# Optimization experiments

Measured on AMD Instinct MI355X. Metric: run time of the kernel, lower is better.

Reference implementation:

```python
import jax, jax.numpy as jnp
import numpy as np

L, D, H, HK, HD, FF = 4, 1024, 16, 8, 64, 3072
WIN = 12          # sliding_window from Krop.__init__
THETA = 1e6       # Qwen3 rope_theta
EPS = 1e-6


def rmsnorm(x, w):
    return x * jax.lax.rsqrt(jnp.mean(x * x, axis=-1, keepdims=True) + EPS) * w


def rope_cos_sin(S):
    inv = 1.0 / (THETA ** (jnp.arange(0, HD, 2, dtype=jnp.float32) / HD))
    ang = jnp.arange(S, dtype=jnp.float32)[:, None] * inv[None, :]  # [S, HD/2]
    emb = jnp.concatenate([ang, ang], axis=-1)                      # [S, HD]
    return jnp.cos(emb), jnp.sin(emb)


def rotate_half(x):
    a, b = jnp.split(x, 2, axis=-1)
    return jnp.concatenate([-b, a], axis=-1)


def apply_rope(x, cos, sin):
    # x: [B,S,h,HD]; cos/sin: [S,HD]
    return x * cos[None, :, None, :] + rotate_half(x) * sin[None, :, None, :]


def setup_inputs() -> dict:
    key = jax.random.key(0)
    ks = jax.random.split(key, 9)
    s = 0.02
    B, S = 4, 1024
    return {
        "inputs_embeds": jax.random.normal(ks[0], (B, S, D), jnp.float32),
        "wq": jax.random.normal(ks[1], (L, D, H * HD), jnp.float32) * s,
        "wk": jax.random.normal(ks[2], (L, D, HK * HD), jnp.float32) * s,
        "wv": jax.random.normal(ks[3], (L, D, HK * HD), jnp.float32) * s,
        "wo": jax.random.normal(ks[4], (L, H * HD, D), jnp.float32) * s,
        "q_norm_w": jnp.ones((L, HD), jnp.float32),
        "k_norm_w": jnp.ones((L, HD), jnp.float32),
        "ln1_w": jnp.ones((L, D), jnp.float32),
        "ln2_w": jnp.ones((L, D), jnp.float32),
        "w_gate": jax.random.normal(ks[5], (L, D, FF), jnp.float32) * s,
        "w_up": jax.random.normal(ks[6], (L, D, FF), jnp.float32) * s,
        "w_down": jax.random.normal(ks[7], (L, FF, D), jnp.float32) * s,
        "norm_w": jnp.ones((D,), jnp.float32),
        "attention_mask": jnp.ones((B, S), jnp.int32),
    }


def reference(inputs_embeds, wq, wk, wv, wo, q_norm_w, k_norm_w, ln1_w, ln2_w,
              w_gate, w_up, w_down, norm_w, attention_mask):
    B, S, _ = inputs_embeds.shape
    pad = attention_mask > 0                                   # [B,S] key-padding
    # _prepare_4d_attention_mask(...) == 0 -> True where attended (NON-causal)
    full_mask = pad[:, None, None, :]                          # [B,1,1,S]
    idx = jnp.arange(S)
    band = jnp.abs(idx[:, None] - idx[None, :]) <= WIN         # tril(triu(.,-W),W)
    sliding_mask = full_mask & band[None, None, :, :]          # [B,1,S,S]

    cos, sin = rope_cos_sin(S)
    scale = 1.0 / np.sqrt(HD)
    neg = jnp.finfo(inputs_embeds.dtype).min

    h = inputs_embeds
    for l in range(L):
        # layer_types alternate: even -> full_attention, odd -> sliding_attention
        mask = full_mask if l % 2 == 0 else sliding_mask
        n = rmsnorm(h, ln1_w[l])
        q = (n @ wq[l]).reshape(B, S, H, HD)
        k = (n @ wk[l]).reshape(B, S, HK, HD)
        v = (n @ wv[l]).reshape(B, S, HK, HD)
        q = apply_rope(rmsnorm(q, q_norm_w[l]), cos, sin)
        k = apply_rope(rmsnorm(k, k_norm_w[l]), cos, sin)
        k = jnp.repeat(k, H // HK, axis=2)                     # GQA expand
        v = jnp.repeat(v, H // HK, axis=2)
        scores = jnp.einsum('bqhd,bkhd->bhqk', q, k) * scale   # eager full scores
        scores = jnp.where(mask, scores, neg)
        p = jax.nn.softmax(scores, axis=-1)
        ctx = jnp.einsum('bhqk,bkhd->bqhd', p, v).reshape(B, S, H * HD)
        h = h + ctx @ wo[l]
        n2 = rmsnorm(h, ln2_w[l])
        h = h + (jax.nn.silu(n2 @ w_gate[l]) * (n2 @ w_up[l])) @ w_down[l]
    return rmsnorm(h, norm_w)
```

## Files before the change

### kernel.cpp

```cpp
#include <hip/hip_runtime.h>

typedef unsigned short u16;
typedef __attribute__((ext_vector_type(8))) short bf16x8;
typedef __attribute__((ext_vector_type(4))) float f32x4;

__device__ __forceinline__ u16 f2bf(float x){
  union { float f; unsigned u; } v; v.f = x;
  unsigned r = v.u + 0x7FFFu + ((v.u >> 16) & 1u);
  return (u16)(r >> 16);
}
__device__ __forceinline__ float bf2f(u16 x){
  union { unsigned u; float f; } v; v.u = ((unsigned)x) << 16;
  return v.f;
}
__device__ __forceinline__ void async16(const u16* g, u16* l){
  __builtin_amdgcn_global_load_lds((const __attribute__((address_space(1))) void*)g,
                                   (__attribute__((address_space(3))) void*)l, 16, 0, 0);
}

__global__ __launch_bounds__(256) void k_transpose_cvt(
    const float* __restrict__ in, u16* __restrict__ out,
    int R, int C, size_t in_ls, size_t out_ls, int c_off){
  __shared__ float tile[32][33];
  in  += (size_t)blockIdx.z * in_ls;
  out += (size_t)blockIdx.z * out_ls;
  int c0 = blockIdx.x * 32 + c_off, r0 = blockIdx.y * 32;
  int tx = threadIdx.x & 31, ty = threadIdx.x >> 5;
  #pragma unroll
  for (int i = 0; i < 32; i += 8)
    tile[ty + i][tx] = in[(size_t)(r0 + ty + i) * C + (c0 + tx)];
  __syncthreads();
  #pragma unroll
  for (int i = 0; i < 32; i += 8)
    out[(size_t)(c0 - c_off + ty + i) * R + (r0 + tx)] = f2bf(tile[tx][ty + i]);
}

__global__ __launch_bounds__(256) void k_rmsnorm(
    const float* __restrict__ x, const float* __restrict__ w,
    void* __restrict__ out, int out_bf16){
  int row = blockIdx.x;
  const float* xr = x + (size_t)row * 1024;
  int tid = threadIdx.x;
  float4 xv = ((const float4*)xr)[tid];
  float ss = xv.x*xv.x + xv.y*xv.y + xv.z*xv.z + xv.w*xv.w;
  #pragma unroll
  for (int off = 32; off >= 1; off >>= 1) ss += __shfl_xor(ss, off);
  __shared__ float red[4];
  if ((tid & 63) == 0) red[tid >> 6] = ss;
  __syncthreads();
  ss = red[0] + red[1] + red[2] + red[3];
  float s = rsqrtf(ss * (1.f/1024.f) + 1e-6f);
  float4 wv = ((const float4*)w)[tid];
  float o0 = xv.x*s*wv.x, o1 = xv.y*s*wv.y, o2 = xv.z*s*wv.z, o3 = xv.w*s*wv.w;
  if (out_bf16){
    u16* orow = (u16*)out + (size_t)row * 1024;
    uint2 pk;
    pk.x = (unsigned)f2bf(o0) | ((unsigned)f2bf(o1) << 16);
    pk.y = (unsigned)f2bf(o2) | ((unsigned)f2bf(o3) << 16);
    *(uint2*)(orow + tid * 4) = pk;
  } else {
    float* orow = (float*)out + (size_t)row * 1024;
    ((float4*)orow)[tid] = make_float4(o0, o1, o2, o3);
  }
}

__global__ __launch_bounds__(256) void k_rope_bf16(
    const float* __restrict__ x, const float* __restrict__ nw,
    u16* __restrict__ dst, int nheads, int src_stride, int dst_stride){
  int gw = (blockIdx.x * 256 + threadIdx.x) >> 6;
  int lane = threadIdx.x & 63;
  int token = gw / nheads;
  int head = gw - token * nheads;
  int pos = token & 1023;
  const float* p = x + (size_t)token * src_stride + head * 64;
  float v = p[lane];
  float ss = v * v;
  #pragma unroll
  for (int off = 32; off >= 1; off >>= 1) ss += __shfl_xor(ss, off);
  float r = rsqrtf(ss * (1.f/64.f) + 1e-6f);
  float xn = v * r * nw[lane];
  float partner = __shfl_xor(xn, 32);
  int i = lane & 31;
  float inv = exp2f(-19.931568569324174f * ((float)(2 * i) * (1.f/64.f)));
  float ang = (float)pos * inv;
  float sn, cs;
  sincosf(ang, &sn, &cs);
  float out = (lane < 32) ? (xn * cs - partner * sn) : (xn * cs + partner * sn);
  dst[(size_t)token * dst_stride + head * 64 + lane] = f2bf(out);
}

__global__ __launch_bounds__(256) void k_gemm(
    const u16* __restrict__ A, const u16* __restrict__ Bt,
    float* __restrict__ Cf, u16* __restrict__ Cb, const float* __restrict__ Aux,
    int M, int N, int K, int epi){
  __shared__ u16 As[128 * 32];
  __shared__ u16 Bs[128 * 32];
  int m0 = blockIdx.x * 128, n0 = blockIdx.y * 128;
  int tid = threadIdx.x;
  int lane = tid & 63, w = tid >> 6;
  int wm = w & 1, wn = w >> 1;
  int quad = lane >> 4, l16 = lane & 15;
  f32x4 acc[4][4];
  #pragma unroll
  for (int a = 0; a < 4; a++)
    #pragma unroll
    for (int b = 0; b < 4; b++) acc[a][b] = (f32x4){0.f, 0.f, 0.f, 0.f};

  for (int k0 = 0; k0 < K; k0 += 32){
    __syncthreads();
    #pragma unroll
    for (int j = 0; j < 2; j++){
      int cb = w * 128 + j * 64;
      int ci = cb + lane;
      int row = ci >> 2, cc = ci & 3;
      async16(A  + (size_t)(m0 + row) * K + k0 + cc * 8, &As[cb * 8]);
      async16(Bt + (size_t)(n0 + row) * K + k0 + cc * 8, &Bs[cb * 8]);
    }
    __syncthreads();
    bf16x8 af[4], bg[4];
    #pragma unroll
    for (int mi = 0; mi < 4; mi++)
      af[mi] = *(const bf16x8*)&As[(wm * 64 + mi * 16 + l16) * 32 + quad * 8];
    #pragma unroll
    for (int ni = 0; ni < 4; ni++)
      bg[ni] = *(const bf16x8*)&Bs[(wn * 64 + ni * 16 + l16) * 32 + quad * 8];
    #pragma unroll
    for (int mi = 0; mi < 4; mi++)
      #pragma unroll
      for (int ni = 0; ni < 4; ni++)
        acc[mi][ni] = __builtin_amdgcn_mfma_f32_16x16x32_bf16(af[mi], bg[ni], acc[mi][ni], 0, 0, 0);
  }
  #pragma unroll
  for (int mi = 0; mi < 4; mi++){
    #pragma unroll
    for (int ni = 0; ni < 4; ni++){
      #pragma unroll
      for (int r = 0; r < 4; r++){
        int row = m0 + wm * 64 + mi * 16 + quad * 4 + r;
        int col = n0 + wn * 64 + ni * 16 + l16;
        size_t idx = (size_t)row * N + col;
        float vv = acc[mi][ni][r];
        if (epi == 0) Cf[idx] = vv;
        else if (epi == 1) Cf[idx] += vv;
        else {
          float g = Aux[idx];
          float sg = g / (1.f + __expf(-g));
          Cb[idx] = f2bf(sg * vv);
        }
      }
    }
  }
}

__global__ __launch_bounds__(256) void k_attn(
    const u16* __restrict__ qh, const u16* __restrict__ kh_,
    const u16* __restrict__ vth, const int* __restrict__ am,
    u16* __restrict__ ctx, int window){
  const int S = 1024, H = 16, HK = 8;
  __shared__ u16 Qs[64 * 72];
  __shared__ u16 Ks[64 * 72];
  __shared__ u16 Vt[64 * 72];
  __shared__ u16 Ps[4][16 * 72];
  __shared__ int Ams[64];
  int b = blockIdx.z, h = blockIdx.y, q0 = blockIdx.x * 64;
  int kvh = h >> 1;
  int tid = threadIdx.x, w = tid >> 6, lane = tid & 63;
  int quad = lane >> 4, l16 = lane & 15;

  #pragma unroll
  for (int i = 0; i < 2; i++){
    int c = tid + i * 256;
    int row = c >> 3, dc = (c & 7) * 8;
    *(uint4*)&Qs[row * 72 + dc] =
        *(const uint4*)(qh + ((size_t)(b * S + q0 + row) * H + h) * 64 + dc);
  }
  __syncthreads();
  bf16x8 aq[2];
  aq[0] = *(const bf16x8*)&Qs[(w * 16 + l16) * 72 + quad * 8];
  aq[1] = *(const bf16x8*)&Qs[(w * 16 + l16) * 72 + 32 + quad * 8];

  f32x4 o[4];
  #pragma unroll
  for (int di = 0; di < 4; di++) o[di] = (f32x4){0.f, 0.f, 0.f, 0.f};
  float m_[4], l_[4];
  #pragma unroll
  for (int r = 0; r < 4; r++){ m_[r] = -1e30f; l_[r] = 0.f; }

  int t0 = 0, t1 = S / 64;
  if (window < S){
    t0 = (q0 > window) ? ((q0 - window) >> 6) : 0;
    int tt = (q0 + 63 + window) / 64 + 1;
    t1 = tt < (S / 64) ? tt : (S / 64);
  }

  for (int t = t0; t < t1; t++){
    __syncthreads();
    #pragma unroll
    for (int i = 0; i < 2; i++){
      int c = tid + i * 256;
      int row = c >> 3, dc = (c & 7) * 8;
      *(uint4*)&Ks[row * 72 + dc] =
          *(const uint4*)(kh_ + ((size_t)(b * S + t * 64 + row) * HK + kvh) * 64 + dc);
      *(uint4*)&Vt[row * 72 + dc] =
          *(const uint4*)(vth + ((size_t)b * 512 + kvh * 64 + row) * S + t * 64 + dc);
    }
    if (tid < 64) Ams[tid] = am[b * S + t * 64 + tid];
    __syncthreads();

    f32x4 sc[4];
    #pragma unroll
    for (int ni = 0; ni < 4; ni++){
      bf16x8 bk0 = *(const bf16x8*)&Ks[(ni * 16 + l16) * 72 + quad * 8];
      bf16x8 bk1 = *(const bf16x8*)&Ks[(ni * 16 + l16) * 72 + 32 + quad * 8];
      sc[ni] = __builtin_amdgcn_mfma_f32_16x16x32_bf16(aq[0], bk0, (f32x4){0.f,0.f,0.f,0.f}, 0, 0, 0);
      sc[ni] = __builtin_amdgcn_mfma_f32_16x16x32_bf16(aq[1], bk1, sc[ni], 0, 0, 0);
    }

    float rowmax[4];
    #pragma unroll
    for (int r = 0; r < 4; r++) rowmax[r] = -1e30f;
    #pragma unroll
    for (int ni = 0; ni < 4; ni++){
      int key = t * 64 + ni * 16 + l16;
      bool kval = Ams[ni * 16 + l16] > 0;
      #pragma unroll
      for (int r = 0; r < 4; r++){
        int qq = q0 + w * 16 + quad * 4 + r;
        int dlt = qq - key; if (dlt < 0) dlt = -dlt;
        bool valid = kval && (dlt <= window);
        float s = valid ? sc[ni][r] * 0.125f : -1e30f;
        sc[ni][r] = s;
        rowmax[r] = fmaxf(rowmax[r], s);
      }
    }
    #pragma unroll
    for (int off = 1; off <= 8; off <<= 1)
      #pragma unroll
      for (int r = 0; r < 4; r++) rowmax[r] = fmaxf(rowmax[r], __shfl_xor(rowmax[r], off));

    float alpha[4], rsum[4];
    #pragma unroll
    for (int r = 0; r < 4; r++){
      float nm = fmaxf(m_[r], rowmax[r]);
      alpha[r] = __expf(m_[r] - nm);
      m_[r] = nm;
      rsum[r] = 0.f;
    }
    #pragma unroll
    for (int ni = 0; ni < 4; ni++){
      #pragma unroll
      for (int r = 0; r < 4; r++){
        float s = sc[ni][r];
        float p = (s == -1e30f) ? 0.f : __expf(s - m_[r]);
        u16 pb = f2bf(p);
        rsum[r] += bf2f(pb);
        Ps[w][(quad * 4 + r) * 72 + ni * 16 + l16] = pb;
      }
    }
    #pragma unroll
    for (int off = 1; off <= 8; off <<= 1)
      #pragma unroll
      for (int r = 0; r < 4; r++) rsum[r] += __shfl_xor(rsum[r], off);
    #pragma unroll
    for (int r = 0; r < 4; r++) l_[r] = l_[r] * alpha[r] + rsum[r];
    #pragma unroll
    for (int di = 0; di < 4; di++)
      #pragma unroll
      for (int r = 0; r < 4; r++) o[di][r] *= alpha[r];

    __syncthreads();

    bf16x8 ap0 = *(const bf16x8*)&Ps[w][l16 * 72 + quad * 8];
    bf16x8 ap1 = *(const bf16x8*)&Ps[w][l16 * 72 + 32 + quad * 8];
    #pragma unroll
    for (int di = 0; di < 4; di++){
      bf16x8 bv0 = *(const bf16x8*)&Vt[(di * 16 + l16) * 72 + quad * 8];
      bf16x8 bv1 = *(const bf16x8*)&Vt[(di * 16 + l16) * 72 + 32 + quad * 8];
      o[di] = __builtin_amdgcn_mfma_f32_16x16x32_bf16(ap0, bv0, o[di], 0, 0, 0);
      o[di] = __builtin_amdgcn_mfma_f32_16x16x32_bf16(ap1, bv1, o[di], 0, 0, 0);
    }
  }

  #pragma unroll
  for (int di = 0; di < 4; di++){
    #pragma unroll
    for (int r = 0; r < 4; r++){
      int qq = q0 + w * 16 + quad * 4 + r;
      float val = o[di][r] / fmaxf(l_[r], 1e-30f);
      ctx[(size_t)(b * S + qq) * 1024 + h * 64 + di * 16 + l16] = f2bf(val);
    }
  }
}

extern "C" void kernel_launch(void* const* d_in, const int* in_sizes, int n_in,
                              void* d_out, int out_size, void* d_ws, size_t ws_size,
                              hipStream_t stream){
  const int L = 4, D = 1024, H = 16, HK = 8, HD = 64, FF = 3072, B = 4, S = 1024;
  const int M = B * S;

  const float* emb = (const float*)d_in[0];
  const float* wq  = (const float*)d_in[1];
  const float* wk  = (const float*)d_in[2];
  const float* wv  = (const float*)d_in[3];
  const float* wo  = (const float*)d_in[4];
  const float* qnw = (const float*)d_in[5];
  const float* knw = (const float*)d_in[6];
  const float* ln1 = (const float*)d_in[7];
  const float* ln2 = (const float*)d_in[8];
  const float* wg  = (const float*)d_in[9];
  const float* wu  = (const float*)d_in[10];
  const float* wd  = (const float*)d_in[11];
  const float* nw  = (const float*)d_in[12];
  const int*   am  = (const int*)d_in[13];
  float* h = (float*)d_out;

  char* ws = (char*)d_ws;
  size_t off = 0;
  auto alloc = [&](size_t bytes) -> void* {
    void* p = ws + off;
    off += (bytes + 255) & ~(size_t)255;
    return p;
  };
  u16* wqkvT = (u16*)alloc((size_t)L * 2048 * D * 2);
  u16* woT = (u16*)alloc((size_t)L * D * (H * HD) * 2);
  u16* wgT = (u16*)alloc((size_t)L * FF * D * 2);
  u16* wuT = (u16*)alloc((size_t)L * FF * D * 2);
  u16* wdT = (u16*)alloc((size_t)L * D * FF * 2);
  u16* nbf  = (u16*)alloc((size_t)M * D * 2);
  u16* ctxb = (u16*)alloc((size_t)M * D * 2);
  float* qkvb = (float*)alloc((size_t)M * 2048 * 4);
  float* gate = (float*)alloc((size_t)M * FF * 4);
  u16* actb = (u16*)alloc((size_t)M * FF * 2);
  (void)ws_size; (void)in_sizes; (void)n_in; (void)out_size;

  u16* qbh = (u16*)gate;
  u16* kbh = (u16*)((char*)gate + (size_t)8 * 1024 * 1024);
  u16* vth = (u16*)((char*)gate + (size_t)12 * 1024 * 1024);

  hipMemcpyAsync(h, emb, (size_t)M * D * 4, hipMemcpyDeviceToDevice, stream);

  k_transpose_cvt<<<dim3(32, 32, L), 256, 0, stream>>>(wq, wqkvT,                      D, 1024, (size_t)D*1024, (size_t)2048*D, 0);
  k_transpose_cvt<<<dim3(16, 32, L), 256, 0, stream>>>(wk, wqkvT + (size_t)1024*D,     D, 512,  (size_t)D*512,  (size_t)2048*D, 0);
  k_transpose_cvt<<<dim3(16, 32, L), 256, 0, stream>>>(wv, wqkvT + (size_t)1536*D,     D, 512,  (size_t)D*512,  (size_t)2048*D, 0);
  k_transpose_cvt<<<dim3(32, 32, L), 256, 0, stream>>>(wo, woT, 1024, D, (size_t)1024*D, (size_t)D*1024, 0);
  k_transpose_cvt<<<dim3(96, 32, L), 256, 0, stream>>>(wg, wgT, D, FF, (size_t)D*FF, (size_t)FF*D, 0);
  k_transpose_cvt<<<dim3(96, 32, L), 256, 0, stream>>>(wu, wuT, D, FF, (size_t)D*FF, (size_t)FF*D, 0);
  k_transpose_cvt<<<dim3(32, 96, L), 256, 0, stream>>>(wd, wdT, FF, D, (size_t)FF*D, (size_t)D*FF, 0);

  for (int l = 0; l < L; l++){
    const u16* wqkvTl = wqkvT + (size_t)l * 2048 * D;
    const u16* woTl = woT + (size_t)l * D * 1024;
    const u16* wgTl = wgT + (size_t)l * FF * D;
    const u16* wuTl = wuT + (size_t)l * FF * D;
    const u16* wdTl = wdT + (size_t)l * D * FF;

    k_rmsnorm<<<M, 256, 0, stream>>>(h, ln1 + l * D, nbf, 1);
    k_gemm<<<dim3(M/128, 2048/128), 256, 0, stream>>>(nbf, wqkvTl, qkvb, nullptr, nullptr, M, 2048, D, 0);
    k_rope_bf16<<<(M * H) / 4, 256, 0, stream>>>(qkvb,        qnw + l * HD, qbh, H,  2048, 1024);
    k_rope_bf16<<<(M * HK) / 4, 256, 0, stream>>>(qkvb + 1024, knw + l * HD, kbh, HK, 2048, 512);
    k_transpose_cvt<<<dim3(16, 32, B), 256, 0, stream>>>(qkvb, vth, S, 2048, (size_t)S*2048, (size_t)512*S, 1536);
    k_attn<<<dim3(S/64, H, B), 256, 0, stream>>>(qbh, kbh, vth, am, ctxb, (l & 1) ? 12 : 2048);
    k_gemm<<<dim3(M/128, 1024/128), 256, 0, stream>>>(ctxb, woTl, h, nullptr, nullptr, M, D, 1024, 1);
    k_rmsnorm<<<M, 256, 0, stream>>>(h, ln2 + l * D, nbf, 1);
    k_gemm<<<dim3(M/128, FF/128), 256, 0, stream>>>(nbf, wgTl, gate, nullptr, nullptr, M, FF, D, 0);
    k_gemm<<<dim3(M/128, FF/128), 256, 0, stream>>>(nbf, wuTl, nullptr, actb, gate, M, FF, D, 2);
    k_gemm<<<dim3(M/128, D/128), 256, 0, stream>>>(actb, wdTl, h, nullptr, nullptr, M, D, FF, 1);
  }
  k_rmsnorm<<<M, 256, 0, stream>>>(h, nw, h, 0);
}
```

Baseline: 1.702 ms.

## Interleave gate/up weights into one GEMM with fused SiLU epilogue; double-buffer GEMM LDS

Gate and up projection weights are transposed into one interleaved matrix in 16-row groups, so a single GEMM computes both. Its epilogue applies SiLU(gate)*up from registers and writes bf16 directly. This removes the fp32 gate buffer write and read-back and one GEMM launch. All GEMMs also gain a two-stage LDS double buffer that prefetches the next K slice while the current one is consumed, at the cost of doubling shared memory per block.

Result: faster. 1.439 ms (-15.5%).

```diff
diff --git a/kernel.cpp b/kernel.cpp
--- a/kernel.cpp
+++ b/kernel.cpp
@@ -20,7 +20,7 @@
 
 __global__ __launch_bounds__(256) void k_transpose_cvt(
     const float* __restrict__ in, u16* __restrict__ out,
-    int R, int C, size_t in_ls, size_t out_ls, int c_off){
+    int R, int C, size_t in_ls, size_t out_ls, int c_off, int grp_stride, int grp_off){
   __shared__ float tile[32][33];
   in  += (size_t)blockIdx.z * in_ls;
   out += (size_t)blockIdx.z * out_ls;
@@ -31,8 +31,11 @@
     tile[ty + i][tx] = in[(size_t)(r0 + ty + i) * C + (c0 + tx)];
   __syncthreads();
   #pragma unroll
-  for (int i = 0; i < 32; i += 8)
-    out[(size_t)(c0 - c_off + ty + i) * R + (r0 + tx)] = f2bf(tile[tx][ty + i]);
+  for (int i = 0; i < 32; i += 8){
+    int r = c0 - c_off + ty + i;
+    int orow = (r >> 4) * grp_stride + grp_off + (r & 15);
+    out[(size_t)orow * R + (r0 + tx)] = f2bf(tile[tx][ty + i]);
+  }
 }
 
 __global__ __launch_bounds__(256) void k_rmsnorm(
@@ -91,10 +94,10 @@
 
 __global__ __launch_bounds__(256) void k_gemm(
     const u16* __restrict__ A, const u16* __restrict__ Bt,
-    float* __restrict__ Cf, u16* __restrict__ Cb, const float* __restrict__ Aux,
+    float* __restrict__ Cf, u16* __restrict__ Cb,
     int M, int N, int K, int epi){
-  __shared__ u16 As[128 * 32];
-  __shared__ u16 Bs[128 * 32];
+  __shared__ u16 As[2][128 * 32];
+  __shared__ u16 Bs[2][128 * 32];
   int m0 = blockIdx.x * 128, n0 = blockIdx.y * 128;
   int tid = threadIdx.x;
   int lane = tid & 63, w = tid >> 6;
@@ -106,46 +109,66 @@
     #pragma unroll
     for (int b = 0; b < 4; b++) acc[a][b] = (f32x4){0.f, 0.f, 0.f, 0.f};
 
-  for (int k0 = 0; k0 < K; k0 += 32){
-    __syncthreads();
+  auto stage = [&](int k0, int buf){
     #pragma unroll
     for (int j = 0; j < 2; j++){
       int cb = w * 128 + j * 64;
       int ci = cb + lane;
       int row = ci >> 2, cc = ci & 3;
-      async16(A  + (size_t)(m0 + row) * K + k0 + cc * 8, &As[cb * 8]);
-      async16(Bt + (size_t)(n0 + row) * K + k0 + cc * 8, &Bs[cb * 8]);
-    }
+      async16(A  + (size_t)(m0 + row) * K + k0 + cc * 8, &As[buf][cb * 8]);
+      async16(Bt + (size_t)(n0 + row) * K + k0 + cc * 8, &Bs[buf][cb * 8]);
+    }
+  };
+
+  stage(0, 0);
+  int cur = 0;
+  for (int k0 = 0; k0 < K; k0 += 32){
     __syncthreads();
+    if (k0 + 32 < K) stage(k0 + 32, cur ^ 1);
     bf16x8 af[4], bg[4];
     #pragma unroll
     for (int mi = 0; mi < 4; mi++)
-      af[mi] = *(const bf16x8*)&As[(wm * 64 + mi * 16 + l16) * 32 + quad * 8];
+      af[mi] = *(const bf16x8*)&As[cur][(wm * 64 + mi * 16 + l16) * 32 + quad * 8];
     #pragma unroll
     for (int ni = 0; ni < 4; ni++)
-      bg[ni] = *(const bf16x8*)&Bs[(wn * 64 + ni * 16 + l16) * 32 + quad * 8];
+      bg[ni] = *(const bf16x8*)&Bs[cur][(wn * 64 + ni * 16 + l16) * 32 + quad * 8];
     #pragma unroll
     for (int mi = 0; mi < 4; mi++)
       #pragma unroll
       for (int ni = 0; ni < 4; ni++)
         acc[mi][ni] = __builtin_amdgcn_mfma_f32_16x16x32_bf16(af[mi], bg[ni], acc[mi][ni], 0, 0, 0);
-  }
-  #pragma unroll
-  for (int mi = 0; mi < 4; mi++){
-    #pragma unroll
-    for (int ni = 0; ni < 4; ni++){
-      #pragma unroll
-      for (int r = 0; r < 4; r++){
-        int row = m0 + wm * 64 + mi * 16 + quad * 4 + r;
-        int col = n0 + wn * 64 + ni * 16 + l16;
-        size_t idx = (size_t)row * N + col;
-        float vv = acc[mi][ni][r];
-        if (epi == 0) Cf[idx] = vv;
-        else if (epi == 1) Cf[idx] += vv;
-        else {
-          float g = Aux[idx];
+    cur ^= 1;
+  }
+
+  if (epi == 3){
+    int cbase = (n0 >> 1) + wn * 32;
+    #pragma unroll
+    for (int mi = 0; mi < 4; mi++){
+      #pragma unroll
+      for (int j = 0; j < 2; j++){
+        #pragma unroll
+        for (int r = 0; r < 4; r++){
+          int row = m0 + wm * 64 + mi * 16 + quad * 4 + r;
+          int col = cbase + j * 16 + l16;
+          float g = acc[mi][2 * j][r];
+          float u = acc[mi][2 * j + 1][r];
           float sg = g / (1.f + __expf(-g));
-          Cb[idx] = f2bf(sg * vv);
+          Cb[(size_t)row * 3072 + col] = f2bf(sg * u);
+        }
+      }
+    }
+  } else {
+    #pragma unroll
+    for (int mi = 0; mi < 4; mi++){
+      #pragma unroll
+      for (int ni = 0; ni < 4; ni++){
+        #pragma unroll
+        for (int r = 0; r < 4; r++){
+          int row = m0 + wm * 64 + mi * 16 + quad * 4 + r;
+          int col = n0 + wn * 64 + ni * 16 + l16;
+          size_t idx = (size_t)row * N + col;
+          if (epi == 0) Cf[idx] = acc[mi][ni][r];
+          else          Cf[idx] += acc[mi][ni][r];
         }
       }
     }
@@ -322,49 +345,44 @@
     return p;
   };
   u16* wqkvT = (u16*)alloc((size_t)L * 2048 * D * 2);
-  u16* woT = (u16*)alloc((size_t)L * D * (H * HD) * 2);
-  u16* wgT = (u16*)alloc((size_t)L * FF * D * 2);
-  u16* wuT = (u16*)alloc((size_t)L * FF * D * 2);
-  u16* wdT = (u16*)alloc((size_t)L * D * FF * 2);
-  u16* nbf  = (u16*)alloc((size_t)M * D * 2);
-  u16* ctxb = (u16*)alloc((size_t)M * D * 2);
+  u16* woT   = (u16*)alloc((size_t)L * D * (H * HD) * 2);
+  u16* wguT  = (u16*)alloc((size_t)L * 2 * FF * D * 2);
+  u16* wdT   = (u16*)alloc((size_t)L * D * FF * 2);
+  u16* nbf   = (u16*)alloc((size_t)M * D * 2);
+  u16* ctxb  = (u16*)alloc((size_t)M * D * 2);
   float* qkvb = (float*)alloc((size_t)M * 2048 * 4);
-  float* gate = (float*)alloc((size_t)M * FF * 4);
-  u16* actb = (u16*)alloc((size_t)M * FF * 2);
+  u16* actb  = (u16*)alloc((size_t)M * FF * 2);
+  u16* qbh   = (u16*)alloc((size_t)M * 1024 * 2);
+  u16* kbh   = (u16*)alloc((size_t)M * 512 * 2);
+  u16* vth   = (u16*)alloc((size_t)B * 512 * S * 2);
   (void)ws_size; (void)in_sizes; (void)n_in; (void)out_size;
 
-  u16* qbh = (u16*)gate;
-  u16* kbh = (u16*)((char*)gate + (size_t)8 * 1024 * 1024);
-  u16* vth = (u16*)((char*)gate + (size_t)12 * 1024 * 1024);
-
   hipMemcpyAsync(h, emb, (size_t)M * D * 4, hipMemcpyDeviceToDevice, stream);
 
-  k_transpose_cvt<<<dim3(32, 32, L), 256, 0, stream>>>(wq, wqkvT,                      D, 1024, (size_t)D*1024, (size_t)2048*D, 0);
-  k_transpose_cvt<<<dim3(16, 32, L), 256, 0, stream>>>(wk, wqkvT + (size_t)1024*D,     D, 512,  (size_t)D*512,  (size_t)2048*D, 0);
-  k_transpose_cvt<<<dim3(16, 32, L), 256, 0, stream>>>(wv, wqkvT + (size_t)1536*D,     D, 512,  (size_t)D*512,  (size_t)2048*D, 0);
-  k_transpose_cvt<<<dim3(32, 32, L), 256, 0, stream>>>(wo, woT, 1024, D, (size_t)1024*D, (size_t)D*1024, 0);
-  k_transpose_cvt<<<dim3(96, 32, L), 256, 0, stream>>>(wg, wgT, D, FF, (size_t)D*FF, (size_t)FF*D, 0);
-  k_transpose_cvt<<<dim3(96, 32, L), 256, 0, stream>>>(wu, wuT, D, FF, (size_t)D*FF, (size_t)FF*D, 0);
-  k_transpose_cvt<<<dim3(32, 96, L), 256, 0, stream>>>(wd, wdT, FF, D, (size_t)FF*D, (size_t)D*FF, 0);
+  k_transpose_cvt<<<dim3(32, 32, L), 256, 0, stream>>>(wq, wqkvT,                  D, 1024, (size_t)D*1024, (size_t)2048*D, 0, 16, 0);
+  k_transpose_cvt<<<dim3(16, 32, L), 256, 0, stream>>>(wk, wqkvT + (size_t)1024*D, D, 512,  (size_t)D*512,  (size_t)2048*D, 0, 16, 0);
+  k_transpose_cvt<<<dim3(16, 32, L), 256, 0, stream>>>(wv, wqkvT + (size_t)1536*D, D, 512,  (size_t)D*512,  (size_t)2048*D, 0, 16, 0);
+  k_transpose_cvt<<<dim3(32, 32, L), 256, 0, stream>>>(wo, woT, 1024, D, (size_t)1024*D, (size_t)D*1024, 0, 16, 0);
+  k_transpose_cvt<<<dim3(96, 32, L), 256, 0, stream>>>(wg, wguT, D, FF, (size_t)D*FF, (size_t)2*FF*D, 0, 32, 0);
+  k_transpose_cvt<<<dim3(96, 32, L), 256, 0, stream>>>(wu, wguT, D, FF, (size_t)D*FF, (size_t)2*FF*D, 0, 32, 16);
+  k_transpose_cvt<<<dim3(32, 96, L), 256, 0, stream>>>(wd, wdT, FF, D, (size_t)FF*D, (size_t)D*FF, 0, 16, 0);
 
   for (int l = 0; l < L; l++){
     const u16* wqkvTl = wqkvT + (size_t)l * 2048 * D;
-    const u16* woTl = woT + (size_t)l * D * 1024;
-    const u16* wgTl = wgT + (size_t)l * FF * D;
-    const u16* wuTl = wuT + (size_t)l * FF * D;
-    const u16* wdTl = wdT + (size_t)l * D * FF;
+    const u16* woTl   = woT  + (size_t)l * D * 1024;
+    const u16* wguTl  = wguT + (size_t)l * 2 * FF * D;
+    const u16* wdTl   = wdT  + (size_t)l * D * FF;
 
     k_rmsnorm<<<M, 256, 0, stream>>>(h, ln1 + l * D, nbf, 1);
-    k_gemm<<<dim3(M/128, 2048/128), 256, 0, stream>>>(nbf, wqkvTl, qkvb, nullptr, nullptr, M, 2048, D, 0);
-    k_rope_bf16<<<(M * H) / 4, 256, 0, stream>>>(qkvb,        qnw + l * HD, qbh, H,  2048, 1024);
+    k_gemm<<<dim3(M/128, 2048/128), 256, 0, stream>>>(nbf, wqkvTl, qkvb, nullptr, M, 2048, D, 0);
+    k_rope_bf16<<<(M * H) / 4, 256, 0, stream>>>(qkvb,         qnw + l * HD, qbh, H,  2048, 1024);
     k_rope_bf16<<<(M * HK) / 4, 256, 0, stream>>>(qkvb + 1024, knw + l * HD, kbh, HK, 2048, 512);
-    k_transpose_cvt<<<dim3(16, 32, B), 256, 0, stream>>>(qkvb, vth, S, 2048, (size_t)S*2048, (size_t)512*S, 1536);
+    k_transpose_cvt<<<dim3(16, 32, B), 256, 0, stream>>>(qkvb, vth, S, 2048, (size_t)S*2048, (size_t)512*S, 1536, 16, 0);
     k_attn<<<dim3(S/64, H, B), 256, 0, stream>>>(qbh, kbh, vth, am, ctxb, (l & 1) ? 12 : 2048);
-    k_gemm<<<dim3(M/128, 1024/128), 256, 0, stream>>>(ctxb, woTl, h, nullptr, nullptr, M, D, 1024, 1);
+    k_gemm<<<dim3(M/128, 1024/128), 256, 0, stream>>>(ctxb, woTl, h, nullptr, M, D, 1024, 1);
     k_rmsnorm<<<M, 256, 0, stream>>>(h, ln2 + l * D, nbf, 1);
-    k_gemm<<<dim3(M/128, FF/128), 256, 0, stream>>>(nbf, wgTl, gate, nullptr, nullptr, M, FF, D, 0);
-    k_gemm<<<dim3(M/128, FF/128), 256, 0, stream>>>(nbf, wuTl, nullptr, actb, gate, M, FF, D, 2);
-    k_gemm<<<dim3(M/128, D/128), 256, 0, stream>>>(actb, wdTl, h, nullptr, nullptr, M, D, FF, 1);
+    k_gemm<<<dim3(M/128, (2*FF)/128), 256, 0, stream>>>(nbf, wguTl, nullptr, actb, M, 2*FF, D, 3);
+    k_gemm<<<dim3(M/128, D/128), 256, 0, stream>>>(actb, wdTl, h, nullptr, M, D, FF, 1);
   }
   k_rmsnorm<<<M, 256, 0, stream>>>(h, nw, h, 0);
 }
```
